# Optimization experiments

Hardware: AMD Instinct MI355X
Metric: run time of the kernel (lower is better)

Reference implementation:

```python
import jax, jax.numpy as jnp
import numpy as np

B, S, D = 1, 2048, 2048          # batch, context_length, embedding_dimension
H, DH = 16, 128                  # num_heads, head_size (= head_output_dimension)
HID = 4 * D                      # SwiGLU hidden dim
LAMBDA_INIT = 0.8
EPS = 1e-6


def setup_inputs() -> dict:
    key = jax.random.key(0)
    ks = jax.random.split(key, 14)
    nrm = lambda k, sh, s=0.02: jax.random.normal(k, sh, jnp.float32) * s
    return {
        "x": jax.random.normal(ks[0], (B, S, D), jnp.float32),
        "g_norm": jnp.ones((D,), jnp.float32),          # shared RMSNorm gain (same layer used twice)
        "Wq1": nrm(ks[1], (H, D, DH)), "Wq2": nrm(ks[2], (H, D, DH)),
        "Wk1": nrm(ks[3], (H, D, DH)), "Wk2": nrm(ks[4], (H, D, DH)),
        "Wv":  nrm(ks[5], (H, D, DH)),
        "lq1": nrm(ks[6], (H, DH), 0.1), "lk1": nrm(ks[7], (H, DH), 0.1),
        "lq2": nrm(ks[8], (H, DH), 0.1), "lk2": nrm(ks[9], (H, DH), 0.1),
        "Wo": nrm(ks[10], (H * DH, D)),
        "W1": nrm(ks[11], (D, HID)), "W2": nrm(ks[12], (D, HID)), "W3": nrm(ks[13], (HID, D)),
    }


def rmsnorm(x, g):
    return x * jax.lax.rsqrt(jnp.mean(x * x, axis=-1, keepdims=True) + EPS) * g


def diff_attention(x, Wq1, Wq2, Wk1, Wk2, Wv, lq1, lk1, lq2, lk2, Wo):
    # per-head projections: [B,S,D] x [H,D,DH] -> [B,H,S,DH]
    proj = lambda W: jnp.einsum('bsd,hde->bhse', x, W)
    q1, q2 = proj(Wq1), proj(Wq2)
    k1, k2 = proj(Wk1), proj(Wk2)
    v = proj(Wv)
    scale = 1.0 / jnp.sqrt(jnp.float32(DH))
    A1 = jax.nn.softmax(jnp.einsum('bhse,bhte->bhst', q1, k1) * scale, axis=-1)
    A2 = jax.nn.softmax(jnp.einsum('bhse,bhte->bhst', q2, k2) * scale, axis=-1)
    # learned per-head lambda: exp(lq1.lk1) - exp(lq2.lk2) + lambda_init
    lam = (jnp.exp(jnp.sum(lq1 * lk1, -1)) - jnp.exp(jnp.sum(lq2 * lk2, -1)) + LAMBDA_INIT)  # [H]
    o = jnp.einsum('bhst,bhte->bhse', A1 - lam[None, :, None, None] * A2, v)  # [B,H,S,DH]
    o = o.transpose(0, 2, 1, 3).reshape(B, S, H * DH)
    return o @ Wo


def reference(x, g_norm, Wq1, Wq2, Wk1, Wk2, Wv, lq1, lk1, lq2, lk2, Wo, W1, W2, W3):
    # Encoder block (dropout=0 -> identity in eval)
    h = rmsnorm(x, g_norm)
    h = diff_attention(h, Wq1, Wq2, Wk1, Wk2, Wv, lq1, lk1, lq2, lk2, Wo) + h
    z = rmsnorm(h, g_norm)
    ffn = (jax.nn.silu(z @ W1) * (z @ W2)) @ W3  # SwiGLU
    return ffn + h
```

## Files before the change

### kernel.cpp

```cpp
#include <hip/hip_runtime.h>

typedef unsigned short u16;
typedef __bf16 bf16x8 __attribute__((ext_vector_type(8)));
typedef float f32x4 __attribute__((ext_vector_type(4)));

#define S_LEN 2048
#define D_DIM 2048
#define NH 16
#define DH 128
#define HID 8192

__device__ __forceinline__ u16 f2bf(float f) {
  unsigned int u = __float_as_uint(f);
  u += 0x7fff + ((u >> 16) & 1);
  return (u16)(u >> 16);
}

__device__ __forceinline__ void gld16(const u16* g, u16* l) {
  __builtin_amdgcn_global_load_lds(
      (const __attribute__((address_space(1))) unsigned int*)g,
      (__attribute__((address_space(3))) unsigned int*)l, 16, 0, 0);
}

__global__ __launch_bounds__(256) void tconv_f2b(const float* __restrict__ in,
                                                 u16* __restrict__ out, int R, int C) {
  __shared__ float tile[32][33];
  size_t boff = (size_t)blockIdx.z * R * C;
  in += boff; out += boff;
  int c0 = blockIdx.x * 32, r0 = blockIdx.y * 32;
  int tx = threadIdx.x, ty = threadIdx.y;
#pragma unroll
  for (int i = 0; i < 32; i += 8) tile[ty + i][tx] = in[(size_t)(r0 + ty + i) * C + c0 + tx];
  __syncthreads();
#pragma unroll
  for (int i = 0; i < 32; i += 8) out[(size_t)(c0 + ty + i) * R + r0 + tx] = f2bf(tile[tx][ty + i]);
}

__global__ __launch_bounds__(256) void tconv_b2b(const u16* __restrict__ in,
                                                 u16* __restrict__ out, int R, int C) {
  __shared__ u16 tile[32][34];
  size_t boff = (size_t)blockIdx.z * R * C;
  in += boff; out += boff;
  int c0 = blockIdx.x * 32, r0 = blockIdx.y * 32;
  int tx = threadIdx.x, ty = threadIdx.y;
#pragma unroll
  for (int i = 0; i < 32; i += 8) tile[ty + i][tx] = in[(size_t)(r0 + ty + i) * C + c0 + tx];
  __syncthreads();
#pragma unroll
  for (int i = 0; i < 32; i += 8) out[(size_t)(c0 + ty + i) * R + r0 + tx] = tile[tx][ty + i];
}

__global__ __launch_bounds__(256) void rmsnorm_kernel(const float* __restrict__ x,
                                                      const float* __restrict__ g,
                                                      float* __restrict__ xf,
                                                      u16* __restrict__ xb) {
  int row = blockIdx.x;
  int t = threadIdx.x;
  const float4* xr = (const float4*)(x + (size_t)row * D_DIM);
  float4 v0 = xr[t];
  float4 v1 = xr[t + 256];
  float ss = v0.x * v0.x + v0.y * v0.y + v0.z * v0.z + v0.w * v0.w +
             v1.x * v1.x + v1.y * v1.y + v1.z * v1.z + v1.w * v1.w;
#pragma unroll
  for (int o = 1; o < 64; o <<= 1) ss += __shfl_xor(ss, o, 64);
  __shared__ float wss[4];
  if ((t & 63) == 0) wss[t >> 6] = ss;
  __syncthreads();
  float tot = wss[0] + wss[1] + wss[2] + wss[3];
  float rs = rsqrtf(tot * (1.0f / D_DIM) + 1e-6f);
  const float4* gr = (const float4*)g;
  float4 g0 = gr[t], g1 = gr[t + 256];
  float4 o0, o1;
  o0.x = v0.x * rs * g0.x; o0.y = v0.y * rs * g0.y; o0.z = v0.z * rs * g0.z; o0.w = v0.w * rs * g0.w;
  o1.x = v1.x * rs * g1.x; o1.y = v1.y * rs * g1.y; o1.z = v1.z * rs * g1.z; o1.w = v1.w * rs * g1.w;
  if (xf) {
    float4* xfr = (float4*)(xf + (size_t)row * D_DIM);
    xfr[t] = o0; xfr[t + 256] = o1;
  }
  ushort4 b0, b1;
  b0.x = f2bf(o0.x); b0.y = f2bf(o0.y); b0.z = f2bf(o0.z); b0.w = f2bf(o0.w);
  b1.x = f2bf(o1.x); b1.y = f2bf(o1.y); b1.z = f2bf(o1.z); b1.w = f2bf(o1.w);
  ushort4* xbr = (ushort4*)(xb + (size_t)row * D_DIM);
  xbr[t] = b0; xbr[t + 256] = b1;
}

__global__ __launch_bounds__(256) void lam_kernel(const float* __restrict__ lq1,
                                                  const float* __restrict__ lk1,
                                                  const float* __restrict__ lq2,
                                                  const float* __restrict__ lk2,
                                                  float* __restrict__ lamw) {
  int t = threadIdx.x;
  int h = t >> 4, i = (t & 15) << 3;
  float d1 = 0.f, d2 = 0.f;
#pragma unroll
  for (int j = 0; j < 8; j++) {
    d1 += lq1[h * DH + i + j] * lk1[h * DH + i + j];
    d2 += lq2[h * DH + i + j] * lk2[h * DH + i + j];
  }
#pragma unroll
  for (int o = 1; o < 16; o <<= 1) { d1 += __shfl_xor(d1, o, 64); d2 += __shfl_xor(d2, o, 64); }
  if ((t & 15) == 0) lamw[h] = __expf(d1) - __expf(d2) + 0.8f;
}

template <int MODE>
__global__ __launch_bounds__(256, (MODE == 2) ? 2 : 3)
void gemm9(const u16* __restrict__ A, const u16* __restrict__ Bt,
           const u16* __restrict__ Bt2, void* __restrict__ Cout,
           const float* __restrict__ res, int N, int K) {
  __shared__ __align__(16) u16 As[3][128 * 32];
  __shared__ __align__(16) u16 Bs[3][128 * 32];
  __shared__ __align__(16) u16 Bs2[(MODE == 2) ? 3 : 1][(MODE == 2) ? 128 * 32 : 8];
  const int t = threadIdx.x;
  const int lane = t & 63, wid = t >> 6;
  const int wm = (wid >> 1) * 64, wn = (wid & 1) * 64;
  const int fr = lane & 15, fq = lane >> 4;
  const int m0 = blockIdx.y * 128, n0 = blockIdx.x * 128;

  f32x4 acc[4][4] = {};
  f32x4 acc2[(MODE == 2) ? 4 : 1][(MODE == 2) ? 4 : 1] = {};

  const int sro = t >> 2;
  const int scol = ((t & 3) ^ (sro & 3)) << 3;
  const u16* aSrc = A + (size_t)(m0 + sro) * K + scol;
  const u16* bSrc = Bt + (size_t)(n0 + sro) * K + scol;
  const u16* b2Src = (MODE == 2) ? (Bt2 + (size_t)(n0 + sro) * K + scol) : nullptr;
  const int NT = K >> 5;

  auto stage = [&](int buf, int kof) {
    gld16(aSrc + kof, &As[buf][t * 8]);
    gld16(aSrc + (size_t)64 * K + kof, &As[buf][2048 + t * 8]);
    gld16(bSrc + kof, &Bs[buf][t * 8]);
    gld16(bSrc + (size_t)64 * K + kof, &Bs[buf][2048 + t * 8]);
    if constexpr (MODE == 2) {
      gld16(b2Src + kof, &Bs2[buf][t * 8]);
      gld16(b2Src + (size_t)64 * K + kof, &Bs2[buf][2048 + t * 8]);
    }
  };

  stage(0, 0);
  stage(1, 32);
  if constexpr (MODE == 2) asm volatile("s_waitcnt vmcnt(6)" ::: "memory");
  else                     asm volatile("s_waitcnt vmcnt(4)" ::: "memory");
  __builtin_amdgcn_s_barrier();

  const int coff = ((fq << 4) ^ ((fr & 3) << 4)) >> 1;

  for (int k = 0; k < NT; ++k) {
    const int r = k % 3, pbuf = (k + 2) % 3;
    const bool pf = (k + 2) < NT;

    bf16x8 af[4], bfr[4];
    bf16x8 b2fr[(MODE == 2) ? 4 : 1];
#pragma unroll
    for (int i = 0; i < 4; ++i)
      af[i] = *(const bf16x8*)&As[r][(wm + i * 16 + fr) * 32 + coff];
#pragma unroll
    for (int j = 0; j < 4; ++j)
      bfr[j] = *(const bf16x8*)&Bs[r][(wn + j * 16 + fr) * 32 + coff];
    if constexpr (MODE == 2) {
#pragma unroll
      for (int j = 0; j < 4; ++j)
        b2fr[j] = *(const bf16x8*)&Bs2[r][(wn + j * 16 + fr) * 32 + coff];
    }

    if (pf) stage(pbuf, (k + 2) << 5);

    __builtin_amdgcn_s_setprio(1);
#pragma unroll
    for (int i = 0; i < 4; ++i)
#pragma unroll
      for (int j = 0; j < 4; ++j)
        acc[i][j] = __builtin_amdgcn_mfma_f32_16x16x32_bf16(af[i], bfr[j], acc[i][j], 0, 0, 0);
    if constexpr (MODE == 2) {
#pragma unroll
      for (int i = 0; i < 4; ++i)
#pragma unroll
        for (int j = 0; j < 4; ++j)
          acc2[i][j] = __builtin_amdgcn_mfma_f32_16x16x32_bf16(af[i], b2fr[j], acc2[i][j], 0, 0, 0);
    }
    __builtin_amdgcn_s_setprio(0);

    if (k + 1 < NT) {
      if (pf) {
        if constexpr (MODE == 2) asm volatile("s_waitcnt vmcnt(6)" ::: "memory");
        else                     asm volatile("s_waitcnt vmcnt(4)" ::: "memory");
      } else {
        asm volatile("s_waitcnt vmcnt(0)" ::: "memory");
      }
      __builtin_amdgcn_s_barrier();
    }
  }

  if constexpr (MODE == 0) {
    const size_t headBase = (size_t)(n0 >> 7) * ((size_t)S_LEN * 128);
#pragma unroll
    for (int i = 0; i < 4; ++i)
#pragma unroll
      for (int j = 0; j < 4; ++j) {
        int row0 = wm + i * 16 + (fq << 2) + m0;
        int colL = wn + j * 16 + fr;
#pragma unroll
        for (int rr = 0; rr < 4; ++rr)
          ((u16*)Cout)[headBase + (size_t)(row0 + rr) * 128 + colL] = f2bf(acc[i][j][rr]);
      }
  } else {
#pragma unroll
    for (int i = 0; i < 4; ++i)
#pragma unroll
      for (int j = 0; j < 4; ++j) {
        int row0 = m0 + wm + i * 16 + (fq << 2);
        int col = n0 + wn + j * 16 + fr;
#pragma unroll
        for (int rr = 0; rr < 4; ++rr) {
          size_t idx = (size_t)(row0 + rr) * N + col;
          float v = acc[i][j][rr];
          if constexpr (MODE == 1) {
            ((float*)Cout)[idx] = v + res[idx];
          } else {
            float g2 = acc2[i][j][rr];
            float sg = v / (1.0f + __expf(-v));
            ((u16*)Cout)[idx] = f2bf(sg * g2);
          }
        }
      }
  }
}

#define LDK 136
#define LDV 40
#define LDP 40

__global__ __launch_bounds__(256) void flash_attn(const u16* __restrict__ q1g,
                                                  const u16* __restrict__ q2g,
                                                  const u16* __restrict__ k1g,
                                                  const u16* __restrict__ k2g,
                                                  const u16* __restrict__ vtg,
                                                  const float* __restrict__ lamw,
                                                  u16* __restrict__ og) {
  __shared__ __align__(16) u16 Ks1[32 * LDK];
  __shared__ __align__(16) u16 Ks2[32 * LDK];
  __shared__ __align__(16) u16 Vs[128 * LDV];
  __shared__ __align__(16) u16 Ps[4 * 2 * 16 * LDP];
  const float scale = 0.08838834764831845f;
  int h = blockIdx.y, qt = blockIdx.x;
  size_t hoff = (size_t)h * S_LEN * DH;
  const u16* q1 = q1g + hoff;
  const u16* q2 = q2g + hoff;
  const u16* k1 = k1g + hoff;
  const u16* k2 = k2g + hoff;
  const u16* vt = vtg + hoff;
  int t = threadIdx.x, wid = t >> 6, lane = t & 63;
  int fr = lane & 15, fq = lane >> 4;
  int qrow = qt * 64 + wid * 16 + fr;
  bf16x8 qf1[4], qf2[4];
#pragma unroll
  for (int ks = 0; ks < 4; ks++) {
    qf1[ks] = *(const bf16x8*)&q1[(size_t)qrow * DH + ks * 32 + fq * 8];
    qf2[ks] = *(const bf16x8*)&q2[(size_t)qrow * DH + ks * 32 + fq * 8];
  }
  bf16x8 ones;
#pragma unroll
  for (int i = 0; i < 8; i++) ones[i] = (__bf16)1.0f;

  f32x4 O1[8] = {};
  f32x4 O2[8] = {};
  f32x4 L1 = {};
  f32x4 L2 = {};
  int skr = t >> 3, skc = (t & 7) << 4;
  int svr = t >> 2, svc = (t & 3) << 3;
  u16* myP1 = &Ps[(wid * 2 + 0) * 16 * LDP];
  u16* myP2 = &Ps[(wid * 2 + 1) * 16 * LDP];

  for (int kt = 0; kt < S_LEN; kt += 32) {
    uint4 ka1 = *(const uint4*)&k1[(size_t)(kt + skr) * DH + skc];
    uint4 kb1 = *(const uint4*)&k1[(size_t)(kt + skr) * DH + skc + 8];
    uint4 ka2 = *(const uint4*)&k2[(size_t)(kt + skr) * DH + skc];
    uint4 kb2 = *(const uint4*)&k2[(size_t)(kt + skr) * DH + skc + 8];
    uint4 va = *(const uint4*)&vt[(size_t)svr * S_LEN + kt + svc];
    uint4 vb = *(const uint4*)&vt[(size_t)(svr + 64) * S_LEN + kt + svc];
    __syncthreads();
    *(uint4*)&Ks1[skr * LDK + skc] = ka1;
    *(uint4*)&Ks1[skr * LDK + skc + 8] = kb1;
    *(uint4*)&Ks2[skr * LDK + skc] = ka2;
    *(uint4*)&Ks2[skr * LDK + skc + 8] = kb2;
    *(uint4*)&Vs[svr * LDV + svc] = va;
    *(uint4*)&Vs[(svr + 64) * LDV + svc] = vb;
    __syncthreads();

    f32x4 s1[2] = {};
    f32x4 s2[2] = {};
#pragma unroll
    for (int nf = 0; nf < 2; nf++)
#pragma unroll
      for (int ks = 0; ks < 4; ks++) {
        bf16x8 b1v = *(const bf16x8*)&Ks1[(nf * 16 + fr) * LDK + ks * 32 + fq * 8];
        s1[nf] = __builtin_amdgcn_mfma_f32_16x16x32_bf16(qf1[ks], b1v, s1[nf], 0, 0, 0);
        bf16x8 b2v = *(const bf16x8*)&Ks2[(nf * 16 + fr) * LDK + ks * 32 + fq * 8];
        s2[nf] = __builtin_amdgcn_mfma_f32_16x16x32_bf16(qf2[ks], b2v, s2[nf], 0, 0, 0);
      }

#pragma unroll
    for (int nf = 0; nf < 2; nf++)
#pragma unroll
      for (int r = 0; r < 4; r++) {
        myP1[(fq * 4 + r) * LDP + nf * 16 + fr] = f2bf(__expf(s1[nf][r] * scale));
        myP2[(fq * 4 + r) * LDP + nf * 16 + fr] = f2bf(__expf(s2[nf][r] * scale));
      }
    asm volatile("s_waitcnt lgkmcnt(0)" ::: "memory");
    bf16x8 pa1 = *(const bf16x8*)&myP1[fr * LDP + fq * 8];
    bf16x8 pa2 = *(const bf16x8*)&myP2[fr * LDP + fq * 8];
    L1 = __builtin_amdgcn_mfma_f32_16x16x32_bf16(pa1, ones, L1, 0, 0, 0);
    L2 = __builtin_amdgcn_mfma_f32_16x16x32_bf16(pa2, ones, L2, 0, 0, 0);
#pragma unroll
    for (int f = 0; f < 8; f++) {
      bf16x8 bv = *(const bf16x8*)&Vs[(f * 16 + fr) * LDV + fq * 8];
      O1[f] = __builtin_amdgcn_mfma_f32_16x16x32_bf16(pa1, bv, O1[f], 0, 0, 0);
      O2[f] = __builtin_amdgcn_mfma_f32_16x16x32_bf16(pa2, bv, O2[f], 0, 0, 0);
    }
  }

  float lam = lamw[h];
#pragma unroll
  for (int r = 0; r < 4; r++) {
    float i1 = 1.0f / L1[r], i2 = lam / L2[r];
#pragma unroll
    for (int f = 0; f < 8; f++) {
      float val = O1[f][r] * i1 - O2[f][r] * i2;
      og[(size_t)(qt * 64 + wid * 16 + fq * 4 + r) * (NH * DH) + h * DH + f * 16 + fr] =
          f2bf(val);
    }
  }
}

extern "C" void kernel_launch(void* const* d_in, const int* in_sizes, int n_in,
                              void* d_out, int out_size, void* d_ws, size_t ws_size,
                              hipStream_t stream) {
  const float* x = (const float*)d_in[0];
  const float* g = (const float*)d_in[1];
  const float* Wq1 = (const float*)d_in[2];
  const float* Wq2 = (const float*)d_in[3];
  const float* Wk1 = (const float*)d_in[4];
  const float* Wk2 = (const float*)d_in[5];
  const float* Wv = (const float*)d_in[6];
  const float* lq1 = (const float*)d_in[7];
  const float* lk1 = (const float*)d_in[8];
  const float* lq2 = (const float*)d_in[9];
  const float* lk2 = (const float*)d_in[10];
  const float* Wo = (const float*)d_in[11];
  const float* W1 = (const float*)d_in[12];
  const float* W2 = (const float*)d_in[13];
  const float* W3 = (const float*)d_in[14];

  char* ws = (char*)d_ws;
  size_t off = 0;
  auto alloc = [&](size_t b) {
    char* p = ws + off;
    off += (b + 255) & ~(size_t)255;
    return p;
  };
  const size_t PROJ_B = (size_t)NH * DH * D_DIM * 2;
  u16* wq1t = (u16*)alloc(PROJ_B);
  u16* wq2t = (u16*)alloc(PROJ_B);
  u16* wk1t = (u16*)alloc(PROJ_B);
  u16* wk2t = (u16*)alloc(PROJ_B);
  u16* wvt = (u16*)alloc(PROJ_B);
  u16* wot = (u16*)alloc((size_t)D_DIM * NH * DH * 2);
  u16* w1t = (u16*)alloc((size_t)HID * D_DIM * 2);
  u16* w2t = (u16*)alloc((size_t)HID * D_DIM * 2);
  u16* w3t = (u16*)alloc((size_t)D_DIM * HID * 2);
  u16* xnb = (u16*)alloc((size_t)S_LEN * D_DIM * 2);
  float* xnf = (float*)alloc((size_t)S_LEN * D_DIM * 4);
  u16* q1b = (u16*)alloc(PROJ_B);
  u16* q2b = (u16*)alloc(PROJ_B);
  u16* k1b = (u16*)alloc(PROJ_B);
  u16* k2b = (u16*)alloc(PROJ_B);
  u16* vb = (u16*)alloc(PROJ_B);
  u16* vtb = (u16*)alloc(PROJ_B);
  float* lamw = (float*)alloc(NH * 4);
  u16* oa = (u16*)alloc((size_t)S_LEN * NH * DH * 2);
  float* hf = (float*)alloc((size_t)S_LEN * D_DIM * 4);
  u16* zb = (u16*)alloc((size_t)S_LEN * D_DIM * 2);
  u16* ffb = (u16*)alloc((size_t)S_LEN * HID * 2);
  if (off > ws_size) return;

  dim3 tpb(32, 8);
  tconv_f2b<<<dim3(DH / 32, D_DIM / 32, NH), tpb, 0, stream>>>(Wq1, wq1t, D_DIM, DH);
  tconv_f2b<<<dim3(DH / 32, D_DIM / 32, NH), tpb, 0, stream>>>(Wq2, wq2t, D_DIM, DH);
  tconv_f2b<<<dim3(DH / 32, D_DIM / 32, NH), tpb, 0, stream>>>(Wk1, wk1t, D_DIM, DH);
  tconv_f2b<<<dim3(DH / 32, D_DIM / 32, NH), tpb, 0, stream>>>(Wk2, wk2t, D_DIM, DH);
  tconv_f2b<<<dim3(DH / 32, D_DIM / 32, NH), tpb, 0, stream>>>(Wv, wvt, D_DIM, DH);
  tconv_f2b<<<dim3(D_DIM / 32, (NH * DH) / 32, 1), tpb, 0, stream>>>(Wo, wot, NH * DH, D_DIM);
  tconv_f2b<<<dim3(HID / 32, D_DIM / 32, 1), tpb, 0, stream>>>(W1, w1t, D_DIM, HID);
  tconv_f2b<<<dim3(HID / 32, D_DIM / 32, 1), tpb, 0, stream>>>(W2, w2t, D_DIM, HID);
  tconv_f2b<<<dim3(D_DIM / 32, HID / 32, 1), tpb, 0, stream>>>(W3, w3t, HID, D_DIM);

  rmsnorm_kernel<<<S_LEN, 256, 0, stream>>>(x, g, xnf, xnb);
  lam_kernel<<<1, 256, 0, stream>>>(lq1, lk1, lq2, lk2, lamw);

  gemm9<0><<<dim3((5 * NH * DH) / 128, S_LEN / 128), 256, 0, stream>>>(
      xnb, wq1t, nullptr, q1b, nullptr, 5 * NH * DH, D_DIM);
  tconv_b2b<<<dim3(DH / 32, S_LEN / 32, NH), tpb, 0, stream>>>(vb, vtb, S_LEN, DH);

  flash_attn<<<dim3(S_LEN / 64, NH), 256, 0, stream>>>(q1b, q2b, k1b, k2b, vtb, lamw, oa);

  gemm9<1><<<dim3(D_DIM / 128, S_LEN / 128), 256, 0, stream>>>(
      oa, wot, nullptr, hf, xnf, D_DIM, NH * DH);
  rmsnorm_kernel<<<S_LEN, 256, 0, stream>>>(hf, g, nullptr, zb);
  gemm9<2><<<dim3(HID / 128, S_LEN / 128), 256, 0, stream>>>(
      zb, w1t, w2t, ffb, nullptr, HID, D_DIM);
  gemm9<1><<<dim3(D_DIM / 128, S_LEN / 128), 256, 0, stream>>>(
      ffb, w3t, nullptr, d_out, hf, D_DIM, HID);
}
```

Before: 888.0 us.

## Split-K the W3 down-projection GEMM and change LDS swizzle pattern

The final FFN down-projection (K=8192) is split into two K halves via a new gemm9 mode with blockIdx.z, writing fp32 partials into a reused workspace buffer. A new combine kernel sums the partials with the residual. The aim is more blocks on the GPU for a 16x16-tile grid, at the cost of extra fp32 traffic for the partials and one more launch. The LDS XOR swizzle is also changed to use row>>1 bits, which alters bank-conflict behaviour in all GEMM modes.

Result: no change. 885.5 us (-0.3%).

```diff
diff --git a/kernel.cpp b/kernel.cpp
--- a/kernel.cpp
+++ b/kernel.cpp
@@ -102,11 +102,25 @@
   if ((t & 15) == 0) lamw[h] = __expf(d1) - __expf(d2) + 0.8f;
 }
 
+__global__ __launch_bounds__(256) void combine2(const float* __restrict__ P,
+                                                const float* __restrict__ res,
+                                                float* __restrict__ out, int n4) {
+  int i = blockIdx.x * 256 + threadIdx.x;
+  if (i >= n4) return;
+  float4 a = ((const float4*)P)[i];
+  float4 b = ((const float4*)P)[i + n4];
+  float4 r = ((const float4*)res)[i];
+  float4 o;
+  o.x = a.x + b.x + r.x; o.y = a.y + b.y + r.y;
+  o.z = a.z + b.z + r.z; o.w = a.w + b.w + r.w;
+  ((float4*)out)[i] = o;
+}
+
 template <int MODE>
 __global__ __launch_bounds__(256, (MODE == 2) ? 2 : 3)
 void gemm9(const u16* __restrict__ A, const u16* __restrict__ Bt,
            const u16* __restrict__ Bt2, void* __restrict__ Cout,
-           const float* __restrict__ res, int N, int K) {
+           const float* __restrict__ res, int N, int K, int ld) {
   __shared__ __align__(16) u16 As[3][128 * 32];
   __shared__ __align__(16) u16 Bs[3][128 * 32];
   __shared__ __align__(16) u16 Bs2[(MODE == 2) ? 3 : 1][(MODE == 2) ? 128 * 32 : 8];
@@ -115,25 +129,26 @@
   const int wm = (wid >> 1) * 64, wn = (wid & 1) * 64;
   const int fr = lane & 15, fq = lane >> 4;
   const int m0 = blockIdx.y * 128, n0 = blockIdx.x * 128;
+  const int kbase = (MODE == 3) ? (int)blockIdx.z * K : 0;
 
   f32x4 acc[4][4] = {};
   f32x4 acc2[(MODE == 2) ? 4 : 1][(MODE == 2) ? 4 : 1] = {};
 
   const int sro = t >> 2;
-  const int scol = ((t & 3) ^ (sro & 3)) << 3;
-  const u16* aSrc = A + (size_t)(m0 + sro) * K + scol;
-  const u16* bSrc = Bt + (size_t)(n0 + sro) * K + scol;
-  const u16* b2Src = (MODE == 2) ? (Bt2 + (size_t)(n0 + sro) * K + scol) : nullptr;
+  const int scol = (((t & 3) ^ ((sro >> 1) & 3)) << 3);
+  const u16* aSrc = A + (size_t)(m0 + sro) * ld + kbase + scol;
+  const u16* bSrc = Bt + (size_t)(n0 + sro) * ld + kbase + scol;
+  const u16* b2Src = (MODE == 2) ? (Bt2 + (size_t)(n0 + sro) * ld + kbase + scol) : nullptr;
   const int NT = K >> 5;
 
   auto stage = [&](int buf, int kof) {
     gld16(aSrc + kof, &As[buf][t * 8]);
-    gld16(aSrc + (size_t)64 * K + kof, &As[buf][2048 + t * 8]);
+    gld16(aSrc + (size_t)64 * ld + kof, &As[buf][2048 + t * 8]);
     gld16(bSrc + kof, &Bs[buf][t * 8]);
-    gld16(bSrc + (size_t)64 * K + kof, &Bs[buf][2048 + t * 8]);
+    gld16(bSrc + (size_t)64 * ld + kof, &Bs[buf][2048 + t * 8]);
     if constexpr (MODE == 2) {
       gld16(b2Src + kof, &Bs2[buf][t * 8]);
-      gld16(b2Src + (size_t)64 * K + kof, &Bs2[buf][2048 + t * 8]);
+      gld16(b2Src + (size_t)64 * ld + kof, &Bs2[buf][2048 + t * 8]);
     }
   };
 
@@ -143,7 +158,7 @@
   else                     asm volatile("s_waitcnt vmcnt(4)" ::: "memory");
   __builtin_amdgcn_s_barrier();
 
-  const int coff = ((fq << 4) ^ ((fr & 3) << 4)) >> 1;
+  const int coff = ((fq ^ ((fr >> 1) & 3)) << 3);
 
   for (int k = 0; k < NT; ++k) {
     const int r = k % 3, pbuf = (k + 2) % 3;
@@ -204,6 +219,8 @@
           ((u16*)Cout)[headBase + (size_t)(row0 + rr) * 128 + colL] = f2bf(acc[i][j][rr]);
       }
   } else {
+    const size_t zoff = (MODE == 3)
+        ? (size_t)blockIdx.z * (size_t)gridDim.y * 128 * (size_t)N : 0;
 #pragma unroll
     for (int i = 0; i < 4; ++i)
 #pragma unroll
@@ -216,6 +233,8 @@
           float v = acc[i][j][rr];
           if constexpr (MODE == 1) {
             ((float*)Cout)[idx] = v + res[idx];
+          } else if constexpr (MODE == 3) {
+            ((float*)Cout)[zoff + idx] = v;
           } else {
             float g2 = acc2[i][j][rr];
             float sg = v / (1.0f + __expf(-v));
@@ -381,6 +400,7 @@
   float* hf = (float*)alloc((size_t)S_LEN * D_DIM * 4);
   u16* zb = (u16*)alloc((size_t)S_LEN * D_DIM * 2);
   u16* ffb = (u16*)alloc((size_t)S_LEN * HID * 2);
+  (void)q2b; (void)k2b;
   if (off > ws_size) return;
 
   dim3 tpb(32, 8);
@@ -398,16 +418,19 @@
   lam_kernel<<<1, 256, 0, stream>>>(lq1, lk1, lq2, lk2, lamw);
 
   gemm9<0><<<dim3((5 * NH * DH) / 128, S_LEN / 128), 256, 0, stream>>>(
-      xnb, wq1t, nullptr, q1b, nullptr, 5 * NH * DH, D_DIM);
+      xnb, wq1t, nullptr, q1b, nullptr, 5 * NH * DH, D_DIM, D_DIM);
   tconv_b2b<<<dim3(DH / 32, S_LEN / 32, NH), tpb, 0, stream>>>(vb, vtb, S_LEN, DH);
 
   flash_attn<<<dim3(S_LEN / 64, NH), 256, 0, stream>>>(q1b, q2b, k1b, k2b, vtb, lamw, oa);
 
   gemm9<1><<<dim3(D_DIM / 128, S_LEN / 128), 256, 0, stream>>>(
-      oa, wot, nullptr, hf, xnf, D_DIM, NH * DH);
+      oa, wot, nullptr, hf, xnf, D_DIM, NH * DH, NH * DH);
   rmsnorm_kernel<<<S_LEN, 256, 0, stream>>>(hf, g, nullptr, zb);
   gemm9<2><<<dim3(HID / 128, S_LEN / 128), 256, 0, stream>>>(
-      zb, w1t, w2t, ffb, nullptr, HID, D_DIM);
-  gemm9<1><<<dim3(D_DIM / 128, S_LEN / 128), 256, 0, stream>>>(
-      ffb, w3t, nullptr, d_out, hf, D_DIM, HID);
-}
+      zb, w1t, w2t, ffb, nullptr, HID, D_DIM, D_DIM);
+  float* Pw3 = (float*)q1b;
+  gemm9<3><<<dim3(D_DIM / 128, S_LEN / 128, 2), 256, 0, stream>>>(
+      ffb, w3t, nullptr, Pw3, nullptr, D_DIM, HID / 2, HID);
+  combine2<<<(S_LEN * D_DIM / 4 + 255) / 256, 256, 0, stream>>>(
+      Pw3, hf, (float*)d_out, S_LEN * D_DIM / 4);
+}
```
